# Kernel optimization log

Measured on AMD Instinct MI355X. Metric: run time of the kernel, lower is better.

The kernel has to match this reference:

```python
import jax, jax.numpy as jnp
import numpy as np

B, NQ, NK, D, DV = 16, 2048, 2048, 128, 128


def setup_inputs() -> dict:
    key = jax.random.key(0)
    kq, kk, kv, kl = jax.random.split(key, 4)
    return {
        "queries": jax.random.normal(kq, (B, NQ, D), dtype=jnp.float32),
        "keys": jax.random.normal(kk, (B, NK, D), dtype=jnp.float32),
        "values": jax.random.normal(kv, (B, NK, DV), dtype=jnp.float32),
        "valid_lens": jax.random.randint(kl, (B,), 1, NK + 1, dtype=jnp.int32),
    }


def reference(queries, keys, values, valid_lens):
    d = queries.shape[-1]
    # scores: [B, NQ, NK]
    scores = jnp.einsum("bqd,bkd->bqk", queries, keys) / jnp.sqrt(jnp.float32(d))
    # mask positions >= valid_len with -1e6 (matches sequence_mask semantics)
    key_pos = jnp.arange(scores.shape[-1], dtype=jnp.int32)  # [NK]
    mask = key_pos[None, None, :] < valid_lens[:, None, None]  # [B,1,NK] -> broadcast over queries
    scores = jnp.where(mask, scores, jnp.float32(-1000000.0))
    attn = jax.nn.softmax(scores, axis=-1)
    # dropout p=0.0 -> identity
    return jnp.einsum("bqk,bkv->bqv", attn, values)
```

## Files before the change

### kernel.cpp

```cpp
#include <hip/hip_runtime.h>


#define B_   16
#define NQ_  2048
#define NK_  2048
#define D_   128
#define DV_  128
#define NTASK_ 512

typedef unsigned short ushort;
typedef __attribute__((ext_vector_type(4))) float          f32x4;
typedef __attribute__((ext_vector_type(8))) __bf16         bf16x8;
typedef __attribute__((ext_vector_type(8))) unsigned short ushort8v;
typedef __attribute__((ext_vector_type(4))) unsigned int   uint4v;

#ifdef __has_builtin
#if __has_builtin(__builtin_amdgcn_cvt_pk_bf16_f32)
#define HAVE_CVT_PK_BF16 1
#endif
#endif

__device__ __forceinline__ ushort f2bf(float f) {
    unsigned u = __builtin_bit_cast(unsigned, f);
    return (ushort)((u + 0x8000u) >> 16);
}
__device__ __forceinline__ unsigned f2bf2(float a, float b) {
#ifdef HAVE_CVT_PK_BF16
    auto t = __builtin_amdgcn_cvt_pk_bf16_f32(a, b);
    return __builtin_bit_cast(unsigned, t);
#else
    return (unsigned)f2bf(a) | ((unsigned)f2bf(b) << 16);
#endif
}
__device__ __forceinline__ float bfpair_sum(unsigned u) {
    float lo = __builtin_bit_cast(float, u << 16);
    float hi = __builtin_bit_cast(float, u & 0xffff0000u);
    return lo + hi;
}
__device__ __forceinline__ void gl_lds16(const ushort* g, ushort* l) {
    __builtin_amdgcn_global_load_lds(
        (const __attribute__((address_space(1))) void*)g,
        (__attribute__((address_space(3))) void*)l, 16, 0, 0);
}

__global__ __launch_bounds__(256) void convert_kv(
    const float* __restrict__ K, const float* __restrict__ V,
    const int* __restrict__ vlen, ushort* __restrict__ Kb, ushort* __restrict__ Vtb)
{
    const int id = blockIdx.x;
    const int b  = id & 15, kt = id >> 4;
    if (kt >= ((vlen[b] + 63) >> 6)) return;
    const int tid = threadIdx.x;
    const float* gK = K + ((size_t)b * NK_ + kt * 64) * D_;
    const float* gV = V + ((size_t)b * NK_ + kt * 64) * DV_;
    ushort* tK = Kb  + ((size_t)b * 32 + kt) * 8192;
    ushort* tV = Vtb + ((size_t)b * 32 + kt) * 8192;

    #pragma unroll
    for (int i = 0; i < 4; ++i) {
        int u = i * 256 + tid;
        int key = u >> 4, d8 = u & 15;
        const float* p = gK + key * D_ + d8 * 8;
        f32x4 a0 = *(const f32x4*)p;
        f32x4 a1 = *(const f32x4*)(p + 4);
        uint4v w;
        w[0] = f2bf2(a0[0], a0[1]); w[1] = f2bf2(a0[2], a0[3]);
        w[2] = f2bf2(a1[0], a1[1]); w[3] = f2bf2(a1[2], a1[3]);
        *(uint4v*)&tK[key * 128 + ((d8 ^ (key & 7)) << 3)] = w;
    }
    #pragma unroll
    for (int i = 0; i < 4; ++i) {
        int u = i * 256 + tid;
        int dv = u & 127, kg = u >> 7;
        const float* vp = gV + (size_t)(kg * 8) * DV_ + dv;
        float v[8];
        #pragma unroll
        for (int j = 0; j < 8; ++j) v[j] = vp[(size_t)j * DV_];
        uint4v w;
        w[0] = f2bf2(v[0], v[1]); w[1] = f2bf2(v[2], v[3]);
        w[2] = f2bf2(v[4], v[5]); w[3] = f2bf2(v[6], v[7]);
        *(uint4v*)&tV[dv * 64 + ((kg ^ (dv & 7)) << 3)] = w;
    }
}

__global__ __launch_bounds__(256, 2) void attn_fwd(
    const float* __restrict__ Q, const int* __restrict__ vlen,
    const ushort* __restrict__ Kb, const ushort* __restrict__ Vtb,
    float* __restrict__ Out)
{
    __shared__ ushort KVbuf[2][16384];
    __shared__ float  lsh[2][64];
    __shared__ int    ssch[16];
    float* Osh = (float*)&KVbuf[0][0];

    const int tid  = threadIdx.x;
    const int w    = tid >> 6;
    const int wq   = w >> 1;
    const int wk   = w & 1;
    const int L    = tid & 63;
    const int col  = L & 15;
    const int quad = L >> 4;

    if (tid < 16) {
        int my = vlen[tid];
        int rank = 0;
        for (int o = 0; o < 16; ++o) {
            int vo = vlen[o];
            if (vo > my || (vo == my && o < tid)) ++rank;
        }
        ssch[rank] = tid;
    }
    __syncthreads();

    const int e     = blockIdx.x;
    const int p_    = e & 7;
    const int b     = ((e >> 3) & 1) ? ssch[15 - p_] : ssch[p_];
    const int qbase = (e >> 4) * 64;
    const int vl    = vlen[b];
    const int ntiles = (vl + 63) >> 6;

    const float qscale = 0.12751743f;
    bf16x8 qf[2][4];
    #pragma unroll
    for (int q16 = 0; q16 < 2; ++q16) {
        const int qrow = qbase + wq * 32 + q16 * 16 + col;
        const float* gQ = Q + ((size_t)b * NQ_ + qrow) * D_;
        #pragma unroll
        for (int c = 0; c < 4; ++c) {
            const float* pp = gQ + c * 32 + quad * 8;
            f32x4 a0 = *(const f32x4*)pp;
            f32x4 a1 = *(const f32x4*)(pp + 4);
            uint4v us;
            us[0] = f2bf2(a0[0] * qscale, a0[1] * qscale);
            us[1] = f2bf2(a0[2] * qscale, a0[3] * qscale);
            us[2] = f2bf2(a1[0] * qscale, a1[1] * qscale);
            us[3] = f2bf2(a1[2] * qscale, a1[3] * qscale);
            qf[q16][c] = __builtin_bit_cast(bf16x8, us);
        }
    }

    f32x4 o[2][8];
    #pragma unroll
    for (int q16 = 0; q16 < 2; ++q16)
        #pragma unroll
        for (int d = 0; d < 8; ++d) o[q16][d] = (f32x4){0.f, 0.f, 0.f, 0.f};
    float l_run[2] = {0.f, 0.f};

    const ushort* tKb = Kb  + (size_t)b * 32 * 8192;
    const ushort* tVb = Vtb + (size_t)b * 32 * 8192;

    #define ISSUE_DMA(KT, BUF)                                               \
        do {                                                                 \
            const ushort* gk = tKb + (size_t)(KT) * 8192;                    \
            const ushort* gv = tVb + (size_t)(KT) * 8192;                    \
            _Pragma("unroll")                                                \
            for (int i = 0; i < 4; ++i) {                                    \
                int off = (i * 256 + tid) * 8;                               \
                gl_lds16(gk + off, &KVbuf[BUF][off]);                        \
                gl_lds16(gv + off, &KVbuf[BUF][8192 + off]);                 \
            }                                                                \
        } while (0)

    ISSUE_DMA(0, 0);

    const int swz = col & 7;

    for (int kt = 0; kt < ntiles; ++kt) {
        const int buf = kt & 1;
        __syncthreads();
        if (kt + 1 < ntiles) ISSUE_DMA(kt + 1, buf ^ 1);

        const ushort* Kt = &KVbuf[buf][0];
        const ushort* Vt = &KVbuf[buf][8192];

        f32x4 s[2][2];
        #pragma unroll
        for (int q16 = 0; q16 < 2; ++q16)
            #pragma unroll
            for (int kc = 0; kc < 2; ++kc) s[q16][kc] = (f32x4){0.f,0.f,0.f,0.f};
        __builtin_amdgcn_s_setprio(1);
        #pragma unroll
        for (int kc = 0; kc < 2; ++kc) {
            const int kbase = (wk * 32 + kc * 16 + col) * 128;
            #pragma unroll
            for (int c = 0; c < 4; ++c) {
                bf16x8 kb = __builtin_bit_cast(bf16x8, *(const ushort8v*)
                    &Kt[kbase + (((c * 4 + quad) ^ swz) << 3)]);
                s[0][kc] = __builtin_amdgcn_mfma_f32_16x16x32_bf16(kb, qf[0][c], s[0][kc], 0, 0, 0);
                s[1][kc] = __builtin_amdgcn_mfma_f32_16x16x32_bf16(kb, qf[1][c], s[1][kc], 0, 0, 0);
            }
        }
        __builtin_amdgcn_s_setprio(0);

        const int rem = vl - kt * 64 - wk * 32;
        if (rem < 32) {
            #pragma unroll
            for (int rr = 0; rr < 4; ++rr) {
                if (quad * 4 + rr >= rem) {
                    s[0][0][rr] = -1e30f; s[1][0][rr] = -1e30f;
                }
                if (16 + quad * 4 + rr >= rem) {
                    s[0][1][rr] = -1e30f; s[1][1][rr] = -1e30f;
                }
            }
        }

        bf16x8 pa[2];
        #pragma unroll
        for (int q16 = 0; q16 < 2; ++q16) {
            unsigned wA = f2bf2(exp2f(s[q16][0][0]), exp2f(s[q16][0][1]));
            unsigned wB = f2bf2(exp2f(s[q16][0][2]), exp2f(s[q16][0][3]));
            unsigned wC = f2bf2(exp2f(s[q16][1][0]), exp2f(s[q16][1][1]));
            unsigned wD = f2bf2(exp2f(s[q16][1][2]), exp2f(s[q16][1][3]));
            l_run[q16] += bfpair_sum(wA) + bfpair_sum(wB) + bfpair_sum(wC) + bfpair_sum(wD);
            asm("v_permlane32_swap_b32 %0, %1" : "+v"(wA), "+v"(wC));
            asm("v_permlane32_swap_b32 %0, %1" : "+v"(wB), "+v"(wD));
            asm("v_permlane16_swap_b32 %0, %1" : "+v"(wA), "+v"(wC));
            asm("v_permlane16_swap_b32 %0, %1" : "+v"(wB), "+v"(wD));
            uint4v pw;
            pw[0] = wA; pw[1] = wB; pw[2] = wC; pw[3] = wD;
            pa[q16] = __builtin_bit_cast(bf16x8, pw);
        }

        __builtin_amdgcn_s_setprio(1);
        #pragma unroll
        for (int dvc = 0; dvc < 8; ++dvc) {
            const int dv = dvc * 16 + col;
            bf16x8 vb = __builtin_bit_cast(bf16x8, *(const ushort8v*)
                &Vt[dv * 64 + (((wk * 4 + quad) ^ swz) << 3)]);
            o[0][dvc] = __builtin_amdgcn_mfma_f32_16x16x32_bf16(pa[0], vb, o[0][dvc], 0, 0, 0);
            o[1][dvc] = __builtin_amdgcn_mfma_f32_16x16x32_bf16(pa[1], vb, o[1][dvc], 0, 0, 0);
        }
        __builtin_amdgcn_s_setprio(0);
    }
    #undef ISSUE_DMA

    #pragma unroll
    for (int q16 = 0; q16 < 2; ++q16) {
        l_run[q16] += __shfl_xor(l_run[q16], 16, 64);
        l_run[q16] += __shfl_xor(l_run[q16], 32, 64);
    }

    __syncthreads();

    if (L < 16) {
        lsh[wk][wq * 32 + L]      = l_run[0];
        lsh[wk][wq * 32 + 16 + L] = l_run[1];
    }
    #pragma unroll
    for (int q16 = 0; q16 < 2; ++q16)
        #pragma unroll
        for (int dvc = 0; dvc < 8; ++dvc)
            #pragma unroll
            for (int rr = 0; rr < 4; ++rr)
                Osh[wk * 8192 + (wq * 32 + q16 * 16 + quad * 4 + rr) * 128 + dvc * 16 + col]
                    = o[q16][dvc][rr];
    __syncthreads();

    float* gO = Out + ((size_t)b * NQ_ + qbase) * DV_;
    #pragma unroll
    for (int i = 0; i < 8; ++i) {
        int idx = i * 256 + tid;
        int row = idx >> 5;
        int dq  = idx & 31;
        f32x4 a0 = *(const f32x4*)&Osh[row * 128 + dq * 4];
        f32x4 a1 = *(const f32x4*)&Osh[8192 + row * 128 + dq * 4];
        float linv = 1.0f / (lsh[0][row] + lsh[1][row]);
        *(f32x4*)&gO[(size_t)row * DV_ + dq * 4] = (a0 + a1) * linv;
    }
}

extern "C" void kernel_launch(void* const* d_in, const int* in_sizes, int n_in,
                              void* d_out, int out_size, void* d_ws, size_t ws_size,
                              hipStream_t stream) {
    const float* Q  = (const float*)d_in[0];
    const float* K  = (const float*)d_in[1];
    const float* V  = (const float*)d_in[2];
    const int*   vl = (const int*)d_in[3];
    float* out = (float*)d_out;

    char* ws = (char*)d_ws;
    ushort* Kbuf = (ushort*)(ws + 4096);
    ushort* Vbuf = Kbuf + (size_t)B_ * 32 * 8192;

    convert_kv<<<dim3(512, 1, 1), dim3(256, 1, 1), 0, stream>>>(K, V, vl, Kbuf, Vbuf);
    attn_fwd<<<dim3(NTASK_, 1, 1), dim3(256, 1, 1), 0, stream>>>(
        Q, vl, Kbuf, Vbuf, out);
}
```

Baseline: 139.3 us.

## Split DV across waves with 512-thread blocks and transpose V via LDS

The attention kernel now runs 512 threads per block, with a new wave index splitting the 128-wide value dimension in two. Each wave keeps half the output accumulators, which lowers register pressure and allows more resident waves, but it duplicates the QK^T and softmax work across the two halves. The block-to-batch mapping is also reordered so consecutive blocks share a batch. The convert kernel now reads V with coalesced row loads and transposes it through padded shared memory instead of using strided global loads.

```diff
diff --git a/kernel.cpp b/kernel.cpp
--- a/kernel.cpp
+++ b/kernel.cpp
@@ -43,10 +43,12 @@
         (__attribute__((address_space(3))) void*)l, 16, 0, 0);
 }
 
+#define VL_STRIDE 132
 __global__ __launch_bounds__(256) void convert_kv(
     const float* __restrict__ K, const float* __restrict__ V,
     const int* __restrict__ vlen, ushort* __restrict__ Kb, ushort* __restrict__ Vtb)
 {
+    __shared__ ushort Vl[64 * VL_STRIDE];
     const int id = blockIdx.x;
     const int b  = id & 15, kt = id >> 4;
     if (kt >= ((vlen[b] + 63) >> 6)) return;
@@ -68,22 +70,39 @@
         w[2] = f2bf2(a1[0], a1[1]); w[3] = f2bf2(a1[2], a1[3]);
         *(uint4v*)&tK[key * 128 + ((d8 ^ (key & 7)) << 3)] = w;
     }
+
     #pragma unroll
     for (int i = 0; i < 4; ++i) {
         int u = i * 256 + tid;
-        int dv = u & 127, kg = u >> 7;
-        const float* vp = gV + (size_t)(kg * 8) * DV_ + dv;
-        float v[8];
-        #pragma unroll
-        for (int j = 0; j < 8; ++j) v[j] = vp[(size_t)j * DV_];
+        int key = u >> 4, d8 = u & 15;
+        const float* p = gV + key * DV_ + d8 * 8;
+        f32x4 a0 = *(const f32x4*)p;
+        f32x4 a1 = *(const f32x4*)(p + 4);
         uint4v w;
-        w[0] = f2bf2(v[0], v[1]); w[1] = f2bf2(v[2], v[3]);
-        w[2] = f2bf2(v[4], v[5]); w[3] = f2bf2(v[6], v[7]);
-        *(uint4v*)&tV[dv * 64 + ((kg ^ (dv & 7)) << 3)] = w;
-    }
-}
-
-__global__ __launch_bounds__(256, 2) void attn_fwd(
+        w[0] = f2bf2(a0[0], a0[1]); w[1] = f2bf2(a0[2], a0[3]);
+        w[2] = f2bf2(a1[0], a1[1]); w[3] = f2bf2(a1[2], a1[3]);
+        *(uint4v*)&Vl[key * VL_STRIDE + d8 * 8] = w;
+    }
+    __syncthreads();
+
+    #pragma unroll
+    for (int i = 0; i < 4; ++i) {
+        int u  = i * 256 + tid;
+        int c  = u & 7, dv = u >> 3;
+        int kg = c ^ (dv & 7);
+        ushort v[8];
+        #pragma unroll
+        for (int j = 0; j < 8; ++j) v[j] = Vl[(kg * 8 + j) * VL_STRIDE + dv];
+        uint4v w;
+        w[0] = (unsigned)v[0] | ((unsigned)v[1] << 16);
+        w[1] = (unsigned)v[2] | ((unsigned)v[3] << 16);
+        w[2] = (unsigned)v[4] | ((unsigned)v[5] << 16);
+        w[3] = (unsigned)v[6] | ((unsigned)v[7] << 16);
+        *(uint4v*)&tV[dv * 64 + c * 8] = w;
+    }
+}
+
+__global__ __launch_bounds__(512, 4) void attn_fwd(
     const float* __restrict__ Q, const int* __restrict__ vlen,
     const ushort* __restrict__ Kb, const ushort* __restrict__ Vtb,
     float* __restrict__ Out)
@@ -95,8 +114,9 @@
 
     const int tid  = threadIdx.x;
     const int w    = tid >> 6;
-    const int wq   = w >> 1;
-    const int wk   = w & 1;
+    const int wq   = w >> 2;
+    const int wk   = (w >> 1) & 1;
+    const int wd   = w & 1;
     const int L    = tid & 63;
     const int col  = L & 15;
     const int quad = L >> 4;
@@ -113,9 +133,9 @@
     __syncthreads();
 
     const int e     = blockIdx.x;
-    const int p_    = e & 7;
-    const int b     = ((e >> 3) & 1) ? ssch[15 - p_] : ssch[p_];
-    const int qbase = (e >> 4) * 64;
+    const int p_    = (e & 255) >> 5;
+    const int b     = (e >> 8) ? ssch[15 - p_] : ssch[p_];
+    const int qbase = (e & 31) * 64;
     const int vl    = vlen[b];
     const int ntiles = (vl + 63) >> 6;
 
@@ -139,11 +159,11 @@
         }
     }
 
-    f32x4 o[2][8];
+    f32x4 o[2][4];
     #pragma unroll
     for (int q16 = 0; q16 < 2; ++q16)
         #pragma unroll
-        for (int d = 0; d < 8; ++d) o[q16][d] = (f32x4){0.f, 0.f, 0.f, 0.f};
+        for (int d = 0; d < 4; ++d) o[q16][d] = (f32x4){0.f, 0.f, 0.f, 0.f};
     float l_run[2] = {0.f, 0.f};
 
     const ushort* tKb = Kb  + (size_t)b * 32 * 8192;
@@ -154,8 +174,8 @@
             const ushort* gk = tKb + (size_t)(KT) * 8192;                    \
             const ushort* gv = tVb + (size_t)(KT) * 8192;                    \
             _Pragma("unroll")                                                \
-            for (int i = 0; i < 4; ++i) {                                    \
-                int off = (i * 256 + tid) * 8;                               \
+            for (int i = 0; i < 2; ++i) {                                    \
+                int off = (i * 512 + tid) * 8;                               \
                 gl_lds16(gk + off, &KVbuf[BUF][off]);                        \
                 gl_lds16(gv + off, &KVbuf[BUF][8192 + off]);                 \
             }                                                                \
@@ -224,8 +244,8 @@
 
         __builtin_amdgcn_s_setprio(1);
         #pragma unroll
-        for (int dvc = 0; dvc < 8; ++dvc) {
-            const int dv = dvc * 16 + col;
+        for (int dvc = 0; dvc < 4; ++dvc) {
+            const int dv = (wd * 4 + dvc) * 16 + col;
             bf16x8 vb = __builtin_bit_cast(bf16x8, *(const ushort8v*)
                 &Vt[dv * 64 + (((wk * 4 + quad) ^ swz) << 3)]);
             o[0][dvc] = __builtin_amdgcn_mfma_f32_16x16x32_bf16(pa[0], vb, o[0][dvc], 0, 0, 0);
@@ -243,24 +263,24 @@
 
     __syncthreads();
 
-    if (L < 16) {
+    if (wd == 0 && L < 16) {
         lsh[wk][wq * 32 + L]      = l_run[0];
         lsh[wk][wq * 32 + 16 + L] = l_run[1];
     }
     #pragma unroll
     for (int q16 = 0; q16 < 2; ++q16)
         #pragma unroll
-        for (int dvc = 0; dvc < 8; ++dvc)
+        for (int dvc = 0; dvc < 4; ++dvc)
             #pragma unroll
             for (int rr = 0; rr < 4; ++rr)
-                Osh[wk * 8192 + (wq * 32 + q16 * 16 + quad * 4 + rr) * 128 + dvc * 16 + col]
-                    = o[q16][dvc][rr];
+                Osh[wk * 8192 + (wq * 32 + q16 * 16 + quad * 4 + rr) * 128
+                    + (wd * 4 + dvc) * 16 + col] = o[q16][dvc][rr];
     __syncthreads();
 
     float* gO = Out + ((size_t)b * NQ_ + qbase) * DV_;
     #pragma unroll
-    for (int i = 0; i < 8; ++i) {
-        int idx = i * 256 + tid;
+    for (int i = 0; i < 4; ++i) {
+        int idx = i * 512 + tid;
         int row = idx >> 5;
         int dq  = idx & 31;
         f32x4 a0 = *(const f32x4*)&Osh[row * 128 + dq * 4];
@@ -284,6 +304,6 @@
     ushort* Vbuf = Kbuf + (size_t)B_ * 32 * 8192;
 
     convert_kv<<<dim3(512, 1, 1), dim3(256, 1, 1), 0, stream>>>(K, V, vl, Kbuf, Vbuf);
-    attn_fwd<<<dim3(NTASK_, 1, 1), dim3(256, 1, 1), 0, stream>>>(
+    attn_fwd<<<dim3(NTASK_, 1, 1), dim3(512, 1, 1), 0, stream>>>(
         Q, vl, Kbuf, Vbuf, out);
 }
```

New measurement: 145.6 us. 4.5% more time.
